# Kernel optimization log

Measured on AMD Instinct MI355X. Metric: run time of the kernel, lower is better.

Reference implementation:

```python
import jax, jax.numpy as jnp
import numpy as np
import math

B, L, H, E, D = 4, 2048, 8, 64, 64
EPS = 1e-6

def _adjust(x):
    # signed power-law (sqrt) then L2-normalize over feature dim
    y = jnp.sign(x) * jnp.sqrt(jnp.abs(x) + EPS)
    return y / (jnp.linalg.norm(y, axis=-1, keepdims=True) + EPS)

def setup_inputs() -> dict:
    key = jax.random.key(0)
    kq, kk, kv, ka = jax.random.split(key, 4)
    queries = jax.random.normal(kq, (B, L, H, E), dtype=jnp.float32)
    keys = jax.random.normal(kk, (B, L, H, E), dtype=jnp.float32)
    values = jax.random.normal(kv, (B, L, H, D), dtype=jnp.float32)
    # TriangularCausalMask: True above the diagonal => masked
    attn_mask = jnp.triu(jnp.ones((1, 1, L, L), dtype=bool), k=1)
    alpha = jax.random.normal(ka, (1,), dtype=jnp.float32) * 0.01
    return {"queries": queries, "keys": keys, "values": values,
            "attn_mask": attn_mask, "alpha": alpha}

def reference(queries, keys, values, attn_mask, alpha):
    Bq, Lq, Hq, Eq = queries.shape
    scale = 1.0 / math.sqrt(Eq)
    # Closed form of torch.autograd.functional.jacobian of
    # sum(einsum('blhe,bshe->bhls', q, k)):
    #   d/dq[b,l,h,e] = sum_s k[b,s,h,e]   (independent of l)
    #   d/dk[b,s,h,e] = sum_l q[b,l,h,e]   (independent of s)
    k_sum = jnp.sum(keys, axis=1, keepdims=True)      # [B,1,H,E]
    q_sum = jnp.sum(queries, axis=1, keepdims=True)   # [B,1,H,E]
    q_adj = _adjust(queries + alpha * k_sum)
    k_adj = _adjust(keys + alpha * q_sum)
    scores = jnp.einsum('blhe,bshe->bhls', q_adj, k_adj)  # [B,H,L,S]
    scores = jnp.where(attn_mask, -jnp.inf, scores)
    A = jax.nn.softmax(scale * scores, axis=-1)  # dropout inactive (eval)
    V = jnp.einsum('bhls,bshd->blhd', A, values)
    return V
```

## Files before the change

kernel.cpp:

```cpp
#include <hip/hip_runtime.h>
#include <hip/hip_bf16.h>
#include <math.h>

#define NB 4
#define NL 2048
#define NH 8
#define NE 64
#define ND 64
#define EPSF 1e-6f
#define CEXP 0.180336881f

typedef __attribute__((ext_vector_type(8))) short bf16x8;
typedef __attribute__((ext_vector_type(4))) short s16x4;
typedef __attribute__((ext_vector_type(4))) float f32x4;

static __device__ __forceinline__ unsigned short bfbits(float x) {
  union { __hip_bfloat16 h; unsigned short u; } c;
  c.h = __float2bfloat16(x);
  return c.u;
}
static __device__ __forceinline__ float b2f(short s) {
  union { float f; unsigned u; } c;
  c.u = ((unsigned)(unsigned short)s) << 16;
  return c.f;
}
static __device__ __forceinline__ float sgnsqrt(float x) {
  return x > 0.f ? sqrtf(x + EPSF) : (x < 0.f ? -sqrtf(-x + EPSF) : 0.f);
}

__global__ __launch_bounds__(256) void sums_kernel(
    const float* __restrict__ q, const float* __restrict__ k,
    float* __restrict__ pq, float* __restrict__ pk,
    __hip_bfloat16* __restrict__ qbf, __hip_bfloat16* __restrict__ kbf) {
  __shared__ f32x4 arr[256];
  int blk = blockIdx.x, t = threadIdx.x;
  int col4 = t & 15;
  int rid0 = blk * 64;
  f32x4 q4[4], k4[4];
#pragma unroll
  for (int j = 0; j < 4; ++j) {
    size_t off = ((size_t)(rid0 + (t >> 4) + 16 * j) * 64 + col4 * 4);
    q4[j] = *(const f32x4*)(q + off);
    k4[j] = *(const f32x4*)(k + off);
  }
  arr[t] = (q4[0] + q4[1]) + (q4[2] + q4[3]);
  __syncthreads();
  if (t < 128) *(f32x4*)(pq + (size_t)blk * 512 + (t >> 4) * 64 + col4 * 4) = arr[t] + arr[t + 128];
  __syncthreads();
  arr[t] = (k4[0] + k4[1]) + (k4[2] + k4[3]);
  __syncthreads();
  if (t < 128) *(f32x4*)(pk + (size_t)blk * 512 + (t >> 4) * 64 + col4 * 4) = arr[t] + arr[t + 128];
#pragma unroll
  for (int j = 0; j < 4; ++j) {
    int rid = rid0 + (t >> 4) + 16 * j;
    int bb = rid >> 14, l = (rid >> 3) & 2047, h = rid & 7;
    size_t o = ((size_t)(bb * 8 + h) * 2048 + l) * 64 + col4 * 4;
    s16x4 uq, uk;
#pragma unroll
    for (int c = 0; c < 4; ++c) {
      uq[c] = (short)bfbits(q4[j][c]);
      uk[c] = (short)bfbits(k4[j][c]);
    }
    *(s16x4*)((char*)qbf + o * 2) = uq;
    *(s16x4*)((char*)kbf + o * 2) = uk;
  }
}

__global__ __launch_bounds__(256) void reduce_kernel(
    const float* __restrict__ pq, const float* __restrict__ pk,
    float* __restrict__ qsumT, float* __restrict__ ksumT) {
  __shared__ float red[512];
  int bh = blockIdx.x;
  int rb = bh >> 3, rh = bh & 7;
  int t = threadIdx.x, e = t & 63, g = t >> 6;
  float sq = 0.f, sk = 0.f;
#pragma unroll 4
  for (int i = 0; i < 64; ++i) {
    size_t sb = (size_t)(rb * 256 + g + 4 * i) * 512 + rh * 64 + e;
    sq += pq[sb];
    sk += pk[sb];
  }
  red[g * 64 + e] = sq;
  __syncthreads();
  if (t < 64) qsumT[bh * 64 + t] = red[t] + red[64 + t] + red[128 + t] + red[192 + t];
  __syncthreads();
  red[g * 64 + e] = sk;
  __syncthreads();
  if (t < 64) ksumT[bh * 64 + t] = red[t] + red[64 + t] + red[128 + t] + red[192 + t];
}

__global__ __launch_bounds__(256) void prep_kernel(
    const __hip_bfloat16* __restrict__ qbf, const __hip_bfloat16* __restrict__ kbf,
    const float* __restrict__ v,
    const float* __restrict__ qsumT, const float* __restrict__ ksumT,
    const float* __restrict__ alpha,
    __hip_bfloat16* __restrict__ qadj, __hip_bfloat16* __restrict__ kadj,
    __hip_bfloat16* __restrict__ vt) {
  __shared__ __align__(16) char sh[9216];
  int t = threadIdx.x;
  if (blockIdx.x < 1024) {
    int bh = blockIdx.x >> 5, l0 = (blockIdx.x & 31) * 64;
    float* aq = (float*)sh;
    float* ak = (float*)(sh + 256);
    if (t < 64) {
      float al = alpha[0];
      aq[t] = al * qsumT[bh * 64 + t];
      ak[t] = al * ksumT[bh * 64 + t];
    }
    __syncthreads();
    int e8 = t & 7, rr = t >> 3;
#pragma unroll
    for (int p = 0; p < 2; ++p) {
      int l = l0 + p * 32 + rr;
      size_t o = ((size_t)bh * 2048 + l) * 64 + e8 * 8;
      bf16x8 xq8 = *(const bf16x8*)((const char*)qbf + o * 2);
      bf16x8 xk8 = *(const bf16x8*)((const char*)kbf + o * 2);
      float yq[8], yk[8];
      float nq = 0.f, nk = 0.f;
#pragma unroll
      for (int c = 0; c < 8; ++c) {
        float xq = b2f(xq8[c]) + ak[e8 * 8 + c];
        float xk = b2f(xk8[c]) + aq[e8 * 8 + c];
        yq[c] = sgnsqrt(xq); nq += yq[c] * yq[c];
        yk[c] = sgnsqrt(xk); nk += yk[c] * yk[c];
      }
#pragma unroll
      for (int m = 1; m < 8; m <<= 1) {
        nq += __shfl_xor(nq, m, 8);
        nk += __shfl_xor(nk, m, 8);
      }
      float iq = 1.f / (sqrtf(nq) + EPSF);
      float ik = 1.f / (sqrtf(nk) + EPSF);
      bf16x8 uq, uk;
#pragma unroll
      for (int c = 0; c < 8; ++c) {
        uq[c] = (short)bfbits(yq[c] * iq);
        uk[c] = (short)bfbits(yk[c] * ik);
      }
      *(bf16x8*)((char*)qadj + o * 2) = uq;
      *(bf16x8*)((char*)kadj + o * 2) = uk;
    }
  } else {
    __hip_bfloat16 (*tile)[68] = (__hip_bfloat16(*)[68])sh;
    int blk = blockIdx.x - 1024;
    int s0 = (blk & 31) * 64;
    int bh = blk >> 5;
    int b = bh >> 3, h = bh & 7;
    {
      int sl = t >> 2, dg = t & 3;
      const float* src = v + (((size_t)b * NL + s0 + sl) * NH + h) * ND + dg * 16;
#pragma unroll
      for (int i = 0; i < 4; ++i) {
        f32x4 f = *(const f32x4*)(src + i * 4);
        tile[sl][dg * 16 + i * 4 + 0] = __float2bfloat16(f[0]);
        tile[sl][dg * 16 + i * 4 + 1] = __float2bfloat16(f[1]);
        tile[sl][dg * 16 + i * 4 + 2] = __float2bfloat16(f[2]);
        tile[sl][dg * 16 + i * 4 + 3] = __float2bfloat16(f[3]);
      }
    }
    __syncthreads();
    {
      int d = t >> 2, sg = t & 3;
      __align__(16) __hip_bfloat16 tmp[16];
#pragma unroll
      for (int i = 0; i < 16; ++i) {
        int c = sg * 16 + i;
        int blk32 = c >> 5, cc = c & 31;
        int cq = cc >> 2, ege = cq >> 1, hi = cq & 1;
        int s_local = blk32 * 32 + hi * 16 + ege * 4 + (cc & 3);
        tmp[i] = tile[s_local][d];
      }
      __hip_bfloat16* dst = vt + ((size_t)bh * ND + d) * NL + s0 + sg * 16;
      *(bf16x8*)(dst) = *(const bf16x8*)&tmp[0];
      *(bf16x8*)(dst + 8) = *(const bf16x8*)&tmp[8];
    }
  }
}

__global__ __launch_bounds__(256, 3) void attn_kernel(const __hip_bfloat16* __restrict__ qadj,
                                                      const __hip_bfloat16* __restrict__ kadj,
                                                      const __hip_bfloat16* __restrict__ vt,
                                                      float* __restrict__ out) {
  __shared__ __align__(16) char lds[49152];
  int bh = blockIdx.x;
  int tile = 63 - (int)blockIdx.y;
  int b = bh >> 3, h = bh & 7;
  int wave = threadIdx.x >> 6, lane = threadIdx.x & 63;
  int qr = lane & 15, eg = lane >> 4;
  int qhalf = wave >> 1, shalf = wave & 1;
  int t0 = tile * 32;
  int nck = (tile >> 1) + 1;
  int qw0 = t0 + qhalf * 16;
  const char* kgb = (const char*)(kadj + (size_t)bh * NL * NE);
  const char* vgb = (const char*)(vt + (size_t)bh * ND * NL);
  const char* qgb = (const char*)(qadj + (size_t)bh * NL * NE);

  int koff[2][2], voff[4];
#pragma unroll
  for (int st2 = 0; st2 < 2; ++st2) {
    int row = shalf * 32 + st2 * 16 + qr;
    int swz = (row & 7) << 4;
    koff[st2][0] = (row * 128 + eg * 16) ^ swz;
    koff[st2][1] = (row * 128 + 64 + eg * 16) ^ swz;
  }
#pragma unroll
  for (int dc = 0; dc < 4; ++dc) {
    int d = dc * 16 + qr;
    voff[dc] = 8192 + ((d * 128 + shalf * 64 + eg * 16) ^ ((d & 7) << 4));
  }
  int src_off[4], dst_off[4];
#pragma unroll
  for (int c = 0; c < 4; ++c) {
    dst_off[c] = (wave * 4 + c) * 1024;
    if (wave < 2) {
      int T = (wave * 4 + c) * 1024 + lane * 16;
      src_off[c] = T ^ (((T >> 7) & 7) << 4);
    } else {
      int T2 = ((wave - 2) * 4 + c) * 1024 + lane * 16;
      int S = T2 ^ (((T2 >> 7) & 7) << 4);
      src_off[c] = (S >> 7) * (NL * 2) + (S & 127);
    }
  }
  const char* sgb = (wave < 2) ? kgb : vgb;
  int smul = (wave < 2) ? 8192 : 128;

  auto STAGE = [&](int bufoff, int ck) {
    const char* sb = sgb + (size_t)ck * smul;
    char* db = lds + bufoff;
#pragma unroll
    for (int c = 0; c < 4; ++c)
      __builtin_amdgcn_global_load_lds(
          (const __attribute__((address_space(1))) unsigned int*)(sb + src_off[c]),
          (__attribute__((address_space(3))) unsigned int*)(db + dst_off[c]),
          16, 0, 0);
  };

  bf16x8 qf0 = *(const bf16x8*)(qgb + (size_t)(qw0 + qr) * 128 + eg * 16);
  bf16x8 qf1 = *(const bf16x8*)(qgb + (size_t)(qw0 + qr) * 128 + 64 + eg * 16);

  f32x4 acc[4];
#pragma unroll
  for (int dc = 0; dc < 4; ++dc) acc[dc] = (f32x4){0.f, 0.f, 0.f, 0.f};
  float srun = 0.f;

  STAGE(0, 0);
  if (nck > 1) STAGE(16384, 1);

  int off_c = 0;
  int off_s = 32768;
#pragma unroll 1
  for (int ck = 0; ck < nck; ++ck) {
    if (ck + 1 < nck) asm volatile("s_waitcnt vmcnt(4)" ::: "memory");
    else              asm volatile("s_waitcnt vmcnt(0)" ::: "memory");
    __builtin_amdgcn_sched_barrier(0);
    __builtin_amdgcn_s_barrier();
    __builtin_amdgcn_sched_barrier(0);
    if (ck + 2 < nck) STAGE(off_s, ck + 2);
    char* base = lds + off_c;

    float p[2][4];
    __builtin_amdgcn_s_setprio(1);
#pragma unroll
    for (int st2 = 0; st2 < 2; ++st2) {
      f32x4 a = (f32x4){0.f, 0.f, 0.f, 0.f};
      bf16x8 k0 = *(const bf16x8*)(base + koff[st2][0]);
      bf16x8 k1 = *(const bf16x8*)(base + koff[st2][1]);
      a = __builtin_amdgcn_mfma_f32_16x16x32_bf16(k0, qf0, a, 0, 0, 0);
      a = __builtin_amdgcn_mfma_f32_16x16x32_bf16(k1, qf1, a, 0, 0, 0);
#pragma unroll
      for (int r = 0; r < 4; ++r) p[st2][r] = a[r];
    }
    __builtin_amdgcn_s_setprio(0);
    if (ck == nck - 1) {
      int sbase = ck * 64 + shalf * 32 + eg * 4;
      int qg = qw0 + qr;
#pragma unroll
      for (int st2 = 0; st2 < 2; ++st2)
#pragma unroll
        for (int r = 0; r < 4; ++r)
          if (sbase + st2 * 16 + r > qg) p[st2][r] = -1e30f;
    }
#pragma unroll
    for (int st2 = 0; st2 < 2; ++st2)
#pragma unroll
      for (int r = 0; r < 4; ++r) p[st2][r] = exp2f((p[st2][r] - 1.0f) * CEXP);
    srun += ((p[0][0] + p[0][1]) + (p[0][2] + p[0][3])) +
            ((p[1][0] + p[1][1]) + (p[1][2] + p[1][3]));

    bf16x8 pb;
#pragma unroll
    for (int j = 0; j < 4; ++j) {
      pb[j] = (short)bfbits(p[0][j]);
      pb[4 + j] = (short)bfbits(p[1][j]);
    }
    __builtin_amdgcn_s_setprio(1);
#pragma unroll
    for (int dc = 0; dc < 4; ++dc) {
      bf16x8 vf = *(const bf16x8*)(base + voff[dc]);
      acc[dc] = __builtin_amdgcn_mfma_f32_16x16x32_bf16(vf, pb, acc[dc], 0, 0, 0);
    }
    __builtin_amdgcn_s_setprio(0);

    off_c = (off_c == 32768) ? 0 : off_c + 16384;
    off_s = (off_s == 32768) ? 0 : off_s + 16384;
  }

  srun += __shfl_xor(srun, 16, 64);
  srun += __shfl_xor(srun, 32, 64);
  __syncthreads();
  if (shalf == 1) {
    float* m = (float*)(lds + qhalf * 4352 + lane * 68);
#pragma unroll
    for (int dc = 0; dc < 4; ++dc)
#pragma unroll
      for (int r = 0; r < 4; ++r) m[dc * 4 + r] = acc[dc][r];
    m[16] = srun;
  }
  __syncthreads();
  if (shalf == 0) {
    const float* m = (const float*)(lds + qhalf * 4352 + lane * 68);
#pragma unroll
    for (int dc = 0; dc < 4; ++dc)
#pragma unroll
      for (int r = 0; r < 4; ++r) acc[dc][r] += m[dc * 4 + r];
    float inv = 1.f / (srun + m[16]);
    int l = qw0 + qr;
    float* orow = out + (((size_t)b * NL + l) * NH + h) * ND;
#pragma unroll
    for (int dc = 0; dc < 4; ++dc) *(f32x4*)(orow + dc * 16 + eg * 4) = acc[dc] * inv;
  }
}

extern "C" void kernel_launch(void* const* d_in, const int* in_sizes, int n_in,
                              void* d_out, int out_size, void* d_ws, size_t ws_size,
                              hipStream_t stream) {
  const float* q = (const float*)d_in[0];
  const float* k = (const float*)d_in[1];
  const float* v = (const float*)d_in[2];
  const float* alpha = (const float*)d_in[4];
  float* out = (float*)d_out;
  char* ws = (char*)d_ws;

  __hip_bfloat16* qadj = (__hip_bfloat16*)(ws);
  __hip_bfloat16* kadj = (__hip_bfloat16*)(ws + 8388608);
  __hip_bfloat16* vt   = (__hip_bfloat16*)(ws + 16777216);
  __hip_bfloat16* qbf  = (__hip_bfloat16*)(ws + 25165824);
  __hip_bfloat16* kbf  = (__hip_bfloat16*)(ws + 33554432);
  float* pq    = (float*)(ws + 41943040);
  float* pk    = (float*)(ws + 41943040 + 2097152);
  float* qsumT = (float*)(ws + 41943040 + 4194304);
  float* ksumT = (float*)(ws + 41943040 + 4194304 + 8192);

  sums_kernel<<<dim3(1024), 256, 0, stream>>>(q, k, pq, pk, qbf, kbf);
  reduce_kernel<<<dim3(32), 256, 0, stream>>>(pq, pk, qsumT, ksumT);
  prep_kernel<<<dim3(2048), 256, 0, stream>>>(qbf, kbf, v, qsumT, ksumT, alpha, qadj, kadj, vt);
  attn_kernel<<<dim3(32, 64), 256, 0, stream>>>(qadj, kadj, vt, out);
}
```

Measured before the change: 160.9 us.

## Double attention query tile to 64 rows with 8-wave blocks sharing K/V staging

The attention kernel now uses 512-thread blocks. Each block covers 64 query rows with four query groups instead of 32 rows with two, so every staged 64-key K/V chunk in LDS serves twice as many queries. This halves the global-to-LDS traffic per query, and each wave issues half as many async loads per stage (with the vmcnt wait adjusted to match). It also packs P into bf16 with v_cvt_pk_bf16_f32 and folds the exp scaling into an fma. The cost is half as many blocks and coarser causal tiles, which may hurt load balance and occupancy.

```diff
diff --git a/kernel.cpp b/kernel.cpp
--- a/kernel.cpp
+++ b/kernel.cpp
@@ -13,6 +13,7 @@
 typedef __attribute__((ext_vector_type(8))) short bf16x8;
 typedef __attribute__((ext_vector_type(4))) short s16x4;
 typedef __attribute__((ext_vector_type(4))) float f32x4;
+typedef __attribute__((ext_vector_type(4))) unsigned int u32x4;
 
 static __device__ __forceinline__ unsigned short bfbits(float x) {
   union { __hip_bfloat16 h; unsigned short u; } c;
@@ -26,6 +27,11 @@
 }
 static __device__ __forceinline__ float sgnsqrt(float x) {
   return x > 0.f ? sqrtf(x + EPSF) : (x < 0.f ? -sqrtf(-x + EPSF) : 0.f);
+}
+static __device__ __forceinline__ unsigned cvtpk(float lo, float hi) {
+  unsigned r;
+  asm("v_cvt_pk_bf16_f32 %0, %1, %2" : "=v"(r) : "v"(lo), "v"(hi));
+  return r;
 }
 
 __global__ __launch_bounds__(256) void sums_kernel(
@@ -177,20 +183,20 @@
   }
 }
 
-__global__ __launch_bounds__(256, 3) void attn_kernel(const __hip_bfloat16* __restrict__ qadj,
+__global__ __launch_bounds__(512, 6) void attn_kernel(const __hip_bfloat16* __restrict__ qadj,
                                                       const __hip_bfloat16* __restrict__ kadj,
                                                       const __hip_bfloat16* __restrict__ vt,
                                                       float* __restrict__ out) {
   __shared__ __align__(16) char lds[49152];
   int bh = blockIdx.x;
-  int tile = 63 - (int)blockIdx.y;
+  int tile = 31 - (int)blockIdx.y;
   int b = bh >> 3, h = bh & 7;
   int wave = threadIdx.x >> 6, lane = threadIdx.x & 63;
   int qr = lane & 15, eg = lane >> 4;
-  int qhalf = wave >> 1, shalf = wave & 1;
-  int t0 = tile * 32;
-  int nck = (tile >> 1) + 1;
-  int qw0 = t0 + qhalf * 16;
+  int qg = wave >> 1, shalf = wave & 1;
+  int t0 = tile * 64;
+  int nck = tile + 1;
+  int qw0 = t0 + qg * 16;
   const char* kgb = (const char*)(kadj + (size_t)bh * NL * NE);
   const char* vgb = (const char*)(vt + (size_t)bh * ND * NL);
   const char* qgb = (const char*)(qadj + (size_t)bh * NL * NE);
@@ -208,27 +214,27 @@
     int d = dc * 16 + qr;
     voff[dc] = 8192 + ((d * 128 + shalf * 64 + eg * 16) ^ ((d & 7) << 4));
   }
-  int src_off[4], dst_off[4];
-#pragma unroll
-  for (int c = 0; c < 4; ++c) {
-    dst_off[c] = (wave * 4 + c) * 1024;
-    if (wave < 2) {
-      int T = (wave * 4 + c) * 1024 + lane * 16;
+  int src_off[2], dst_off[2];
+#pragma unroll
+  for (int c = 0; c < 2; ++c) {
+    dst_off[c] = (wave * 2 + c) * 1024;
+    if (wave < 4) {
+      int T = (wave * 2 + c) * 1024 + lane * 16;
       src_off[c] = T ^ (((T >> 7) & 7) << 4);
     } else {
-      int T2 = ((wave - 2) * 4 + c) * 1024 + lane * 16;
+      int T2 = ((wave - 4) * 2 + c) * 1024 + lane * 16;
       int S = T2 ^ (((T2 >> 7) & 7) << 4);
       src_off[c] = (S >> 7) * (NL * 2) + (S & 127);
     }
   }
-  const char* sgb = (wave < 2) ? kgb : vgb;
-  int smul = (wave < 2) ? 8192 : 128;
+  const char* sgb = (wave < 4) ? kgb : vgb;
+  int smul = (wave < 4) ? 8192 : 128;
 
   auto STAGE = [&](int bufoff, int ck) {
     const char* sb = sgb + (size_t)ck * smul;
     char* db = lds + bufoff;
 #pragma unroll
-    for (int c = 0; c < 4; ++c)
+    for (int c = 0; c < 2; ++c)
       __builtin_amdgcn_global_load_lds(
           (const __attribute__((address_space(1))) unsigned int*)(sb + src_off[c]),
           (__attribute__((address_space(3))) unsigned int*)(db + dst_off[c]),
@@ -250,7 +256,7 @@
   int off_s = 32768;
 #pragma unroll 1
   for (int ck = 0; ck < nck; ++ck) {
-    if (ck + 1 < nck) asm volatile("s_waitcnt vmcnt(4)" ::: "memory");
+    if (ck + 1 < nck) asm volatile("s_waitcnt vmcnt(2)" ::: "memory");
     else              asm volatile("s_waitcnt vmcnt(0)" ::: "memory");
     __builtin_amdgcn_sched_barrier(0);
     __builtin_amdgcn_s_barrier();
@@ -258,46 +264,50 @@
     if (ck + 2 < nck) STAGE(off_s, ck + 2);
     char* base = lds + off_c;
 
-    float p[2][4];
+    f32x4 s0a = (f32x4){0.f, 0.f, 0.f, 0.f};
+    f32x4 s1a = (f32x4){0.f, 0.f, 0.f, 0.f};
     __builtin_amdgcn_s_setprio(1);
-#pragma unroll
-    for (int st2 = 0; st2 < 2; ++st2) {
-      f32x4 a = (f32x4){0.f, 0.f, 0.f, 0.f};
-      bf16x8 k0 = *(const bf16x8*)(base + koff[st2][0]);
-      bf16x8 k1 = *(const bf16x8*)(base + koff[st2][1]);
-      a = __builtin_amdgcn_mfma_f32_16x16x32_bf16(k0, qf0, a, 0, 0, 0);
-      a = __builtin_amdgcn_mfma_f32_16x16x32_bf16(k1, qf1, a, 0, 0, 0);
-#pragma unroll
-      for (int r = 0; r < 4; ++r) p[st2][r] = a[r];
+    {
+      bf16x8 k00 = *(const bf16x8*)(base + koff[0][0]);
+      bf16x8 k01 = *(const bf16x8*)(base + koff[0][1]);
+      bf16x8 k10 = *(const bf16x8*)(base + koff[1][0]);
+      bf16x8 k11 = *(const bf16x8*)(base + koff[1][1]);
+      s0a = __builtin_amdgcn_mfma_f32_16x16x32_bf16(k00, qf0, s0a, 0, 0, 0);
+      s0a = __builtin_amdgcn_mfma_f32_16x16x32_bf16(k01, qf1, s0a, 0, 0, 0);
+      s1a = __builtin_amdgcn_mfma_f32_16x16x32_bf16(k10, qf0, s1a, 0, 0, 0);
+      s1a = __builtin_amdgcn_mfma_f32_16x16x32_bf16(k11, qf1, s1a, 0, 0, 0);
     }
     __builtin_amdgcn_s_setprio(0);
     if (ck == nck - 1) {
       int sbase = ck * 64 + shalf * 32 + eg * 4;
-      int qg = qw0 + qr;
-#pragma unroll
-      for (int st2 = 0; st2 < 2; ++st2)
-#pragma unroll
-        for (int r = 0; r < 4; ++r)
-          if (sbase + st2 * 16 + r > qg) p[st2][r] = -1e30f;
-    }
-#pragma unroll
-    for (int st2 = 0; st2 < 2; ++st2)
-#pragma unroll
-      for (int r = 0; r < 4; ++r) p[st2][r] = exp2f((p[st2][r] - 1.0f) * CEXP);
-    srun += ((p[0][0] + p[0][1]) + (p[0][2] + p[0][3])) +
-            ((p[1][0] + p[1][1]) + (p[1][2] + p[1][3]));
-
-    bf16x8 pb;
-#pragma unroll
-    for (int j = 0; j < 4; ++j) {
-      pb[j] = (short)bfbits(p[0][j]);
-      pb[4 + j] = (short)bfbits(p[1][j]);
-    }
+      int qg_ = qw0 + qr;
+#pragma unroll
+      for (int r = 0; r < 4; ++r) {
+        if (sbase + r > qg_) s0a[r] = -1e30f;
+        if (sbase + 16 + r > qg_) s1a[r] = -1e30f;
+      }
+    }
+#pragma unroll
+    for (int r = 0; r < 4; ++r) {
+      s0a[r] = exp2f(fmaf(s0a[r], CEXP, -CEXP));
+      s1a[r] = exp2f(fmaf(s1a[r], CEXP, -CEXP));
+    }
+    srun += ((s0a[0] + s0a[1]) + (s0a[2] + s0a[3])) +
+            ((s1a[0] + s1a[1]) + (s1a[2] + s1a[3]));
+
+    u32x4 pbw;
+    pbw[0] = cvtpk(s0a[0], s0a[1]);
+    pbw[1] = cvtpk(s0a[2], s0a[3]);
+    pbw[2] = cvtpk(s1a[0], s1a[1]);
+    pbw[3] = cvtpk(s1a[2], s1a[3]);
+    union { u32x4 u; bf16x8 v; } pbu;
+    pbu.u = pbw;
+
     __builtin_amdgcn_s_setprio(1);
 #pragma unroll
     for (int dc = 0; dc < 4; ++dc) {
       bf16x8 vf = *(const bf16x8*)(base + voff[dc]);
-      acc[dc] = __builtin_amdgcn_mfma_f32_16x16x32_bf16(vf, pb, acc[dc], 0, 0, 0);
+      acc[dc] = __builtin_amdgcn_mfma_f32_16x16x32_bf16(vf, pbu.v, acc[dc], 0, 0, 0);
     }
     __builtin_amdgcn_s_setprio(0);
 
@@ -309,7 +319,7 @@
   srun += __shfl_xor(srun, 32, 64);
   __syncthreads();
   if (shalf == 1) {
-    float* m = (float*)(lds + qhalf * 4352 + lane * 68);
+    float* m = (float*)(lds + qg * 4352 + lane * 68);
 #pragma unroll
     for (int dc = 0; dc < 4; ++dc)
 #pragma unroll
@@ -318,7 +328,7 @@
   }
   __syncthreads();
   if (shalf == 0) {
-    const float* m = (const float*)(lds + qhalf * 4352 + lane * 68);
+    const float* m = (const float*)(lds + qg * 4352 + lane * 68);
 #pragma unroll
     for (int dc = 0; dc < 4; ++dc)
 #pragma unroll
@@ -354,5 +364,5 @@
   sums_kernel<<<dim3(1024), 256, 0, stream>>>(q, k, pq, pk, qbf, kbf);
   reduce_kernel<<<dim3(32), 256, 0, stream>>>(pq, pk, qsumT, ksumT);
   prep_kernel<<<dim3(2048), 256, 0, stream>>>(qbf, kbf, v, qsumT, ksumT, alpha, qadj, kadj, vt);
-  attn_kernel<<<dim3(32, 64), 256, 0, stream>>>(qadj, kadj, vt, out);
-}
+  attn_kernel<<<dim3(32, 32), 512, 0, stream>>>(qadj, kadj, vt, out);
+}
```

After: 154.9 us. 1.04x faster.

## Replace LDS-staged attention with direct register loads and chunked V layout

Applied to the files above, without the earlier changes.

The attention kernel no longer stages K and V through LDS with global_load_lds and barriers. Each wave now loads its K and V fragments straight from global memory into registers, double-buffered across 64-key chunks, and owns a 16-query slice over the full key range, which removes the cross-wave LDS reduction. The prep kernel writes V transposed in 32-key chunks so each fragment load is contiguous, and bf16 packing uses v_cvt_pk_bf16_f32. In exchange, K/V tiles are no longer shared through LDS, so global and L2 traffic goes up, register pressure rises, and the causal load balance changes with 512-thread blocks.

```diff
diff --git a/kernel.cpp b/kernel.cpp
--- a/kernel.cpp
+++ b/kernel.cpp
@@ -13,6 +13,7 @@
 typedef __attribute__((ext_vector_type(8))) short bf16x8;
 typedef __attribute__((ext_vector_type(4))) short s16x4;
 typedef __attribute__((ext_vector_type(4))) float f32x4;
+typedef __attribute__((ext_vector_type(4))) unsigned int u32x4;
 
 static __device__ __forceinline__ unsigned short bfbits(float x) {
   union { __hip_bfloat16 h; unsigned short u; } c;
@@ -26,6 +27,11 @@
 }
 static __device__ __forceinline__ float sgnsqrt(float x) {
   return x > 0.f ? sqrtf(x + EPSF) : (x < 0.f ? -sqrtf(-x + EPSF) : 0.f);
+}
+static __device__ __forceinline__ unsigned cvtpk(float lo, float hi) {
+  unsigned r;
+  asm("v_cvt_pk_bf16_f32 %0, %1, %2" : "=v"(r) : "v"(lo), "v"(hi));
+  return r;
 }
 
 __global__ __launch_bounds__(256) void sums_kernel(
@@ -170,165 +176,117 @@
         int s_local = blk32 * 32 + hi * 16 + ege * 4 + (cc & 3);
         tmp[i] = tile[s_local][d];
       }
-      __hip_bfloat16* dst = vt + ((size_t)bh * ND + d) * NL + s0 + sg * 16;
+      int chunk = (s0 >> 5) + (sg >> 1);
+      __hip_bfloat16* dst = vt + (((size_t)bh * 64 + chunk) * 64 + d) * 32 + (sg & 1) * 16;
       *(bf16x8*)(dst) = *(const bf16x8*)&tmp[0];
       *(bf16x8*)(dst + 8) = *(const bf16x8*)&tmp[8];
     }
   }
 }
 
-__global__ __launch_bounds__(256, 3) void attn_kernel(const __hip_bfloat16* __restrict__ qadj,
-                                                      const __hip_bfloat16* __restrict__ kadj,
-                                                      const __hip_bfloat16* __restrict__ vt,
-                                                      float* __restrict__ out) {
-  __shared__ __align__(16) char lds[49152];
+__global__ __launch_bounds__(512) void attn_kernel(const __hip_bfloat16* __restrict__ qadj,
+                                                   const __hip_bfloat16* __restrict__ kadj,
+                                                   const __hip_bfloat16* __restrict__ vtt,
+                                                   float* __restrict__ out) {
   int bh = blockIdx.x;
-  int tile = 63 - (int)blockIdx.y;
+  int tile = 15 - (int)blockIdx.y;
   int b = bh >> 3, h = bh & 7;
   int wave = threadIdx.x >> 6, lane = threadIdx.x & 63;
   int qr = lane & 15, eg = lane >> 4;
-  int qhalf = wave >> 1, shalf = wave & 1;
-  int t0 = tile * 32;
-  int nck = (tile >> 1) + 1;
-  int qw0 = t0 + qhalf * 16;
-  const char* kgb = (const char*)(kadj + (size_t)bh * NL * NE);
-  const char* vgb = (const char*)(vt + (size_t)bh * ND * NL);
+  int qw0 = tile * 128 + wave * 16;
+  int nck = (qw0 >> 6) + 1;
+  int qglob = qw0 + qr;
+  const char* kgb = (const char*)(kadj + (size_t)bh * NL * NE) + qr * 128 + eg * 16;
+  const char* vgb = (const char*)(vtt + (size_t)bh * 64 * 64 * 32) + qr * 64 + eg * 16;
   const char* qgb = (const char*)(qadj + (size_t)bh * NL * NE);
 
-  int koff[2][2], voff[4];
-#pragma unroll
-  for (int st2 = 0; st2 < 2; ++st2) {
-    int row = shalf * 32 + st2 * 16 + qr;
-    int swz = (row & 7) << 4;
-    koff[st2][0] = (row * 128 + eg * 16) ^ swz;
-    koff[st2][1] = (row * 128 + 64 + eg * 16) ^ swz;
-  }
-#pragma unroll
-  for (int dc = 0; dc < 4; ++dc) {
-    int d = dc * 16 + qr;
-    voff[dc] = 8192 + ((d * 128 + shalf * 64 + eg * 16) ^ ((d & 7) << 4));
-  }
-  int src_off[4], dst_off[4];
-#pragma unroll
-  for (int c = 0; c < 4; ++c) {
-    dst_off[c] = (wave * 4 + c) * 1024;
-    if (wave < 2) {
-      int T = (wave * 4 + c) * 1024 + lane * 16;
-      src_off[c] = T ^ (((T >> 7) & 7) << 4);
-    } else {
-      int T2 = ((wave - 2) * 4 + c) * 1024 + lane * 16;
-      int S = T2 ^ (((T2 >> 7) & 7) << 4);
-      src_off[c] = (S >> 7) * (NL * 2) + (S & 127);
-    }
-  }
-  const char* sgb = (wave < 2) ? kgb : vgb;
-  int smul = (wave < 2) ? 8192 : 128;
-
-  auto STAGE = [&](int bufoff, int ck) {
-    const char* sb = sgb + (size_t)ck * smul;
-    char* db = lds + bufoff;
-#pragma unroll
-    for (int c = 0; c < 4; ++c)
-      __builtin_amdgcn_global_load_lds(
-          (const __attribute__((address_space(1))) unsigned int*)(sb + src_off[c]),
-          (__attribute__((address_space(3))) unsigned int*)(db + dst_off[c]),
-          16, 0, 0);
-  };
-
-  bf16x8 qf0 = *(const bf16x8*)(qgb + (size_t)(qw0 + qr) * 128 + eg * 16);
-  bf16x8 qf1 = *(const bf16x8*)(qgb + (size_t)(qw0 + qr) * 128 + 64 + eg * 16);
+  bf16x8 qf0 = *(const bf16x8*)(qgb + (size_t)qglob * 128 + eg * 16);
+  bf16x8 qf1 = *(const bf16x8*)(qgb + (size_t)qglob * 128 + 64 + eg * 16);
 
   f32x4 acc[4];
 #pragma unroll
   for (int dc = 0; dc < 4; ++dc) acc[dc] = (f32x4){0.f, 0.f, 0.f, 0.f};
   float srun = 0.f;
 
-  STAGE(0, 0);
-  if (nck > 1) STAGE(16384, 1);
-
-  int off_c = 0;
-  int off_s = 32768;
-#pragma unroll 1
-  for (int ck = 0; ck < nck; ++ck) {
-    if (ck + 1 < nck) asm volatile("s_waitcnt vmcnt(4)" ::: "memory");
-    else              asm volatile("s_waitcnt vmcnt(0)" ::: "memory");
-    __builtin_amdgcn_sched_barrier(0);
-    __builtin_amdgcn_s_barrier();
-    __builtin_amdgcn_sched_barrier(0);
-    if (ck + 2 < nck) STAGE(off_s, ck + 2);
-    char* base = lds + off_c;
-
-    float p[2][4];
+  bf16x8 kfA[4][2], vfA[2][4], kfB[4][2], vfB[2][4];
+
+  auto LOADF = [&](bf16x8 (&kf)[4][2], bf16x8 (&vf)[2][4], int ck) {
+    const char* kp = kgb + (size_t)ck * 8192;
+    const char* vp = vgb + (size_t)ck * 8192;
+#pragma unroll
+    for (int st = 0; st < 4; ++st) {
+      kf[st][0] = *(const bf16x8*)(kp + st * 2048);
+      kf[st][1] = *(const bf16x8*)(kp + st * 2048 + 64);
+    }
+#pragma unroll
+    for (int pp = 0; pp < 2; ++pp)
+#pragma unroll
+      for (int dc = 0; dc < 4; ++dc)
+        vf[pp][dc] = *(const bf16x8*)(vp + pp * 4096 + dc * 1024);
+  };
+
+  auto COMPUTE = [&](bf16x8 (&kf)[4][2], bf16x8 (&vf)[2][4], int ck) {
+    f32x4 sA[4];
     __builtin_amdgcn_s_setprio(1);
 #pragma unroll
-    for (int st2 = 0; st2 < 2; ++st2) {
+    for (int st = 0; st < 4; ++st) {
       f32x4 a = (f32x4){0.f, 0.f, 0.f, 0.f};
-      bf16x8 k0 = *(const bf16x8*)(base + koff[st2][0]);
-      bf16x8 k1 = *(const bf16x8*)(base + koff[st2][1]);
-      a = __builtin_amdgcn_mfma_f32_16x16x32_bf16(k0, qf0, a, 0, 0, 0);
-      a = __builtin_amdgcn_mfma_f32_16x16x32_bf16(k1, qf1, a, 0, 0, 0);
-#pragma unroll
-      for (int r = 0; r < 4; ++r) p[st2][r] = a[r];
+      a = __builtin_amdgcn_mfma_f32_16x16x32_bf16(kf[st][0], qf0, a, 0, 0, 0);
+      a = __builtin_amdgcn_mfma_f32_16x16x32_bf16(kf[st][1], qf1, a, 0, 0, 0);
+      sA[st] = a;
     }
     __builtin_amdgcn_s_setprio(0);
     if (ck == nck - 1) {
-      int sbase = ck * 64 + shalf * 32 + eg * 4;
-      int qg = qw0 + qr;
-#pragma unroll
-      for (int st2 = 0; st2 < 2; ++st2)
+      int sb = ck * 64 + eg * 4;
+#pragma unroll
+      for (int st = 0; st < 4; ++st)
 #pragma unroll
         for (int r = 0; r < 4; ++r)
-          if (sbase + st2 * 16 + r > qg) p[st2][r] = -1e30f;
-    }
-#pragma unroll
-    for (int st2 = 0; st2 < 2; ++st2)
-#pragma unroll
-      for (int r = 0; r < 4; ++r) p[st2][r] = exp2f((p[st2][r] - 1.0f) * CEXP);
-    srun += ((p[0][0] + p[0][1]) + (p[0][2] + p[0][3])) +
-            ((p[1][0] + p[1][1]) + (p[1][2] + p[1][3]));
-
-    bf16x8 pb;
-#pragma unroll
-    for (int j = 0; j < 4; ++j) {
-      pb[j] = (short)bfbits(p[0][j]);
-      pb[4 + j] = (short)bfbits(p[1][j]);
-    }
+          if (sb + st * 16 + r > qglob) sA[st][r] = -1e30f;
+    }
+#pragma unroll
+    for (int st = 0; st < 4; ++st)
+#pragma unroll
+      for (int r = 0; r < 4; ++r) sA[st][r] = exp2f(fmaf(sA[st][r], CEXP, -CEXP));
+    srun += (((sA[0][0] + sA[0][1]) + (sA[0][2] + sA[0][3])) +
+             ((sA[1][0] + sA[1][1]) + (sA[1][2] + sA[1][3]))) +
+            (((sA[2][0] + sA[2][1]) + (sA[2][2] + sA[2][3])) +
+             ((sA[3][0] + sA[3][1]) + (sA[3][2] + sA[3][3])));
+    union { u32x4 u; bf16x8 v; } p0, p1;
+    p0.u[0] = cvtpk(sA[0][0], sA[0][1]);
+    p0.u[1] = cvtpk(sA[0][2], sA[0][3]);
+    p0.u[2] = cvtpk(sA[1][0], sA[1][1]);
+    p0.u[3] = cvtpk(sA[1][2], sA[1][3]);
+    p1.u[0] = cvtpk(sA[2][0], sA[2][1]);
+    p1.u[1] = cvtpk(sA[2][2], sA[2][3]);
+    p1.u[2] = cvtpk(sA[3][0], sA[3][1]);
+    p1.u[3] = cvtpk(sA[3][2], sA[3][3]);
     __builtin_amdgcn_s_setprio(1);
 #pragma unroll
     for (int dc = 0; dc < 4; ++dc) {
-      bf16x8 vf = *(const bf16x8*)(base + voff[dc]);
-      acc[dc] = __builtin_amdgcn_mfma_f32_16x16x32_bf16(vf, pb, acc[dc], 0, 0, 0);
+      acc[dc] = __builtin_amdgcn_mfma_f32_16x16x32_bf16(vf[0][dc], p0.v, acc[dc], 0, 0, 0);
+      acc[dc] = __builtin_amdgcn_mfma_f32_16x16x32_bf16(vf[1][dc], p1.v, acc[dc], 0, 0, 0);
     }
     __builtin_amdgcn_s_setprio(0);
-
-    off_c = (off_c == 32768) ? 0 : off_c + 16384;
-    off_s = (off_s == 32768) ? 0 : off_s + 16384;
-  }
+  };
+
+  LOADF(kfA, vfA, 0);
+  int ck = 0;
+#pragma unroll 1
+  for (; ck + 2 <= nck; ck += 2) {
+    LOADF(kfB, vfB, ck + 1);
+    COMPUTE(kfA, vfA, ck);
+    if (ck + 2 < nck) LOADF(kfA, vfA, ck + 2);
+    COMPUTE(kfB, vfB, ck + 1);
+  }
+  if (ck < nck) COMPUTE(kfA, vfA, ck);
 
   srun += __shfl_xor(srun, 16, 64);
   srun += __shfl_xor(srun, 32, 64);
-  __syncthreads();
-  if (shalf == 1) {
-    float* m = (float*)(lds + qhalf * 4352 + lane * 68);
-#pragma unroll
-    for (int dc = 0; dc < 4; ++dc)
-#pragma unroll
-      for (int r = 0; r < 4; ++r) m[dc * 4 + r] = acc[dc][r];
-    m[16] = srun;
-  }
-  __syncthreads();
-  if (shalf == 0) {
-    const float* m = (const float*)(lds + qhalf * 4352 + lane * 68);
-#pragma unroll
-    for (int dc = 0; dc < 4; ++dc)
-#pragma unroll
-      for (int r = 0; r < 4; ++r) acc[dc][r] += m[dc * 4 + r];
-    float inv = 1.f / (srun + m[16]);
-    int l = qw0 + qr;
-    float* orow = out + (((size_t)b * NL + l) * NH + h) * ND;
-#pragma unroll
-    for (int dc = 0; dc < 4; ++dc) *(f32x4*)(orow + dc * 16 + eg * 4) = acc[dc] * inv;
-  }
+  float inv = 1.f / srun;
+  float* orow = out + (((size_t)b * NL + qglob) * NH + h) * ND;
+#pragma unroll
+  for (int dc = 0; dc < 4; ++dc) *(f32x4*)(orow + dc * 16 + eg * 4) = acc[dc] * inv;
 }
 
 extern "C" void kernel_launch(void* const* d_in, const int* in_sizes, int n_in,
@@ -354,5 +312,5 @@
   sums_kernel<<<dim3(1024), 256, 0, stream>>>(q, k, pq, pk, qbf, kbf);
   reduce_kernel<<<dim3(32), 256, 0, stream>>>(pq, pk, qsumT, ksumT);
   prep_kernel<<<dim3(2048), 256, 0, stream>>>(qbf, kbf, v, qsumT, ksumT, alpha, qadj, kadj, vt);
-  attn_kernel<<<dim3(32, 64), 256, 0, stream>>>(qadj, kadj, vt, out);
-}
+  attn_kernel<<<dim3(32, 16), 512, 0, stream>>>(qadj, kadj, vt, out);
+}
```

Measured after the change: 216.1 us. 34.3% more time.
